# Kernel optimization log

Measured on AMD Instinct MI355X. Metric: run time of the kernel, lower is better.

The kernel has to match this reference:

```python
import jax, jax.numpy as jnp
import numpy as np

B, T, F, H = 8192, 96, 64, 256


def setup_inputs() -> dict:
    key = jax.random.key(0)
    ks = jax.random.split(key, 8)
    s = 0.05
    return {
        "decoder_feature": jax.random.normal(ks[0], (B, T, F), jnp.float32),
        "init_state": jax.random.normal(ks[1], (B, H), jnp.float32),
        "decoder_init_input": jax.random.normal(ks[2], (B, 1), jnp.float32),
        "kernel": jax.random.normal(ks[3], (1 + F, 3 * H), jnp.float32) * s,
        "recurrent_kernel": jax.random.normal(ks[4], (H, 3 * H), jnp.float32) * s,
        "input_bias": jnp.zeros((3 * H,), jnp.float32),
        "recurrent_bias": jnp.zeros((3 * H,), jnp.float32),
        "dense_w": jax.random.normal(ks[5], (H, 1), jnp.float32) * s,
        "dense_b": jnp.zeros((1,), jnp.float32),
        "predict_seq_length": T,
    }


def reference(decoder_feature, init_state, decoder_init_input, kernel,
              recurrent_kernel, input_bias, recurrent_bias, dense_w, dense_b,
              predict_seq_length):
    # teacher=None, use_attention=False path of Decoder2.forward.
    # Keras GRUCell (reset_after=True) recurrence, scanned over time.
    feats = jnp.swapaxes(decoder_feature[:, :predict_seq_length, :], 0, 1)  # [T,B,F]

    def step(carry, feat_t):
        prev_out, h = carry                                   # [B,1], [B,H]
        x = jnp.concatenate([prev_out, feat_t], axis=-1)      # [B,1+F]
        mx = x @ kernel + input_bias                          # [B,3H]
        mh = h @ recurrent_kernel + recurrent_bias            # [B,3H]
        xz, xr, xh = jnp.split(mx, 3, axis=-1)
        hz, hr, hh = jnp.split(mh, 3, axis=-1)
        z = jax.nn.sigmoid(xz + hz)
        r = jax.nn.sigmoid(xr + hr)
        cand = jnp.tanh(xh + r * hh)
        h_new = z * h + (1.0 - z) * cand
        out = h_new @ dense_w + dense_b                       # [B,1]
        return (out, h_new), out

    _, outs = jax.lax.scan(step, (decoder_init_input, init_state), feats)
    return jnp.swapaxes(outs, 0, 1)                           # [B,T,1]
```

## Files before the change

### kernel.cpp

```cpp
#include <hip/hip_runtime.h>


#define Bdim 8192
#define Tdim 96
#define Fdim 64
#define Hdim 256
#define BM   32
#define XS   72
#define HS   264
#define OS   97

typedef __attribute__((ext_vector_type(8))) short s16x8;
typedef __attribute__((ext_vector_type(4))) float f32x4;

#define MFMA __builtin_amdgcn_mfma_f32_16x16x32_bf16

__device__ __forceinline__ unsigned short f2bf(float f) {
    union { float f; unsigned u; } v; v.f = f;
    unsigned r = v.u + 0x7FFFu + ((v.u >> 16) & 1u);
    return (unsigned short)(r >> 16);
}

__device__ __forceinline__ float sigm_fast(float x) {
    return __builtin_amdgcn_rcpf(1.0f + __expf(-x));
}
__device__ __forceinline__ float tanh_fast(float x) {
    return 1.0f - 2.0f * __builtin_amdgcn_rcpf(1.0f + __expf(2.0f * x));
}

__global__ void prep_swz(const float* __restrict__ Wk, const float* __restrict__ Wr,
                         unsigned short* __restrict__ sW) {
    int idx = blockIdx.x * blockDim.x + threadIdx.x;
    if (idx >= 480 * 64) return;
    int lane = idx & 63, f = idx >> 6;
    int n2 = f & 1;
    int g  = (f >> 1) % 3;
    int kt = (f / 6) % 10;
    int w  = f / 60;
    int q = lane >> 4, cc = lane & 15;
    int n = g * 256 + w * 32 + n2 * 16 + cc;
    unsigned short* d = sW + (size_t)idx * 8;
#pragma unroll
    for (int j = 0; j < 8; ++j) {
        float v;
        if (kt < 8) v = Wr[(size_t)(kt * 32 + q * 8 + j) * 768 + n];
        else        v = Wk[(size_t)(1 + (kt - 8) * 32 + q * 8 + j) * 768 + n];
        d[j] = f2bf(v);
    }
}

__launch_bounds__(1024)
__global__ void gru_mfma11(
    const float* __restrict__ feat,
    const float* __restrict__ init_state,
    const float* __restrict__ init_inp,
    const unsigned short* __restrict__ sW,
    const float* __restrict__ Wk,
    const float* __restrict__ ib, const float* __restrict__ rb,
    const float* __restrict__ dw, const float* __restrict__ db,
    float* __restrict__ out)
{
    __shared__ __align__(16) unsigned short xs[2][BM * XS];
    __shared__ __align__(16) unsigned short hs[2][BM * HS];
    __shared__ float wpart[2][16][BM];
    __shared__ float outbuf[BM * OS];

    const int tid  = threadIdx.x;
    const int lane = tid & 63;
    const int wv   = tid >> 6;
    const int q    = lane >> 4;
    const int c    = lane & 15;
    const int b0   = blockIdx.x * BM;
    const int col  = wv * 16 + c;

    const float bz   = ib[col]       + rb[col];
    const float brr  = ib[256 + col] + rb[256 + col];
    const float bxh  = ib[512 + col];
    const float bhh  = rb[512 + col];
    const float wk0z = Wk[col];
    const float wk0r = Wk[256 + col];
    const float wk0h = Wk[512 + col];
    const float dwv  = dw[col];
    const float dbv  = db[0];

    float hreg[2][4];
#pragma unroll
    for (int mt = 0; mt < 2; ++mt)
#pragma unroll
        for (int i = 0; i < 4; ++i) {
            int row = mt * 16 + q * 4 + i;
            float v = init_state[(size_t)(b0 + row) * Hdim + col];
            hreg[mt][i] = v;
            hs[0][row * HS + col] = f2bf(v);
        }

    if (tid < 16 * BM) {
        int ww = tid >> 5, r = tid & 31;
        wpart[1][ww][r] = (ww == 0) ? (init_inp[b0 + r] - dbv) : 0.0f;
    }

    {
        int r = tid >> 5, fi = tid & 31;
        float2 f = *(const float2*)&feat[((size_t)(b0 + r) * Tdim + 0) * Fdim + fi * 2];
        ushort2 p; p.x = f2bf(f.x); p.y = f2bf(f.y);
        *(ushort2*)&xs[0][r * XS + fi * 2] = p;
    }

    const unsigned short* wp0 =
        sW + ((size_t)(wv >> 1) * 60 + (wv & 1)) * 512 + lane * 8;

    __syncthreads();

    for (int t = 0; t < Tdim; ++t) {
        const unsigned short* hsp = hs[t & 1];
        const unsigned short* xsp = xs[t & 1];

        f32x4 az[2], ar[2], ax[2], ah[2];
#pragma unroll
        for (int mt = 0; mt < 2; ++mt) {
            az[mt] = (f32x4)0.0f; ar[mt] = (f32x4)0.0f;
            ax[mt] = (f32x4)0.0f; ah[mt] = (f32x4)0.0f;
        }

#pragma unroll
        for (int kt = 0; kt < 10; ++kt) {
            s16x8 b0f = *(const s16x8*)(wp0 + (size_t)(kt * 3 + 0) * 1024);
            s16x8 b1f = *(const s16x8*)(wp0 + (size_t)(kt * 3 + 1) * 1024);
            s16x8 b2f = *(const s16x8*)(wp0 + (size_t)(kt * 3 + 2) * 1024);
            s16x8 a0, a1;
            if (kt < 8) {
                a0 = *(const s16x8*)&hsp[c * HS + kt * 32 + q * 8];
                a1 = *(const s16x8*)&hsp[(16 + c) * HS + kt * 32 + q * 8];
            } else {
                a0 = *(const s16x8*)&xsp[c * XS + (kt - 8) * 32 + q * 8];
                a1 = *(const s16x8*)&xsp[(16 + c) * XS + (kt - 8) * 32 + q * 8];
            }
            az[0] = MFMA(a0, b0f, az[0], 0, 0, 0);
            az[1] = MFMA(a1, b0f, az[1], 0, 0, 0);
            ar[0] = MFMA(a0, b1f, ar[0], 0, 0, 0);
            ar[1] = MFMA(a1, b1f, ar[1], 0, 0, 0);
            if (kt < 8) {
                ah[0] = MFMA(a0, b2f, ah[0], 0, 0, 0);
                ah[1] = MFMA(a1, b2f, ah[1], 0, 0, 0);
            } else {
                ax[0] = MFMA(a0, b2f, ax[0], 0, 0, 0);
                ax[1] = MFMA(a1, b2f, ax[1], 0, 0, 0);
            }
        }

        float2 fnext;
        int fr = tid >> 5, ffi = tid & 31;
        if (t + 1 < Tdim)
            fnext = *(const float2*)&feat[((size_t)(b0 + fr) * Tdim + (t + 1)) * Fdim + ffi * 2];

        __syncthreads();

        float s;
        {
            int r = lane & 31;
            s = dbv;
            const float (*wp)[BM] = wpart[(t - 1) & 1];
#pragma unroll
            for (int ww = 0; ww < 16; ++ww) s += wp[ww][r];
            if (t > 0 && wv == 0 && lane < 32) outbuf[r * OS + (t - 1)] = s;
        }

        unsigned short* hsn = hs[(t + 1) & 1];
#pragma unroll
        for (int mt = 0; mt < 2; ++mt)
#pragma unroll
            for (int i = 0; i < 4; ++i) {
                float pv = __shfl(s, mt * 16 + q * 4 + i, 64);
                float zz = sigm_fast(az[mt][i] + bz + pv * wk0z);
                float rr = sigm_fast(ar[mt][i] + brr + pv * wk0r);
                float cd = tanh_fast(ax[mt][i] + bxh + pv * wk0h +
                                     rr * (ah[mt][i] + bhh));
                float hn = zz * hreg[mt][i] + (1.0f - zz) * cd;
                hreg[mt][i] = hn;
                hsn[(mt * 16 + q * 4 + i) * HS + col] = f2bf(hn);
                float sp = hn * dwv;
                sp += __shfl_xor(sp, 1, 64);
                sp += __shfl_xor(sp, 2, 64);
                sp += __shfl_xor(sp, 4, 64);
                sp += __shfl_xor(sp, 8, 64);
                if (c == 0) wpart[t & 1][wv][mt * 16 + q * 4 + i] = sp;
            }

        if (t + 1 < Tdim) {
            ushort2 p; p.x = f2bf(fnext.x); p.y = f2bf(fnext.y);
            *(ushort2*)&xs[(t + 1) & 1][fr * XS + ffi * 2] = p;
        }
        __syncthreads();
    }

    {
        int r = lane & 31;
        float s = dbv;
        const float (*wp)[BM] = wpart[(Tdim - 1) & 1];
#pragma unroll
        for (int ww = 0; ww < 16; ++ww) s += wp[ww][r];
        if (wv == 0 && lane < 32) outbuf[r * OS + (Tdim - 1)] = s;
    }
    __syncthreads();

    for (int i = tid; i < BM * Tdim; i += 1024) {
        int r = i / Tdim, tt = i - r * Tdim;
        out[(size_t)b0 * Tdim + i] = outbuf[r * OS + tt];
    }
}

extern "C" void kernel_launch(void* const* d_in, const int* in_sizes, int n_in,
                              void* d_out, int out_size, void* d_ws, size_t ws_size,
                              hipStream_t stream) {
    const float* feat       = (const float*)d_in[0];
    const float* init_state = (const float*)d_in[1];
    const float* init_inp   = (const float*)d_in[2];
    const float* Wk         = (const float*)d_in[3];
    const float* Wr         = (const float*)d_in[4];
    const float* ib         = (const float*)d_in[5];
    const float* rb         = (const float*)d_in[6];
    const float* dw         = (const float*)d_in[7];
    const float* db         = (const float*)d_in[8];
    float* out              = (float*)d_out;

    unsigned short* sW = (unsigned short*)d_ws;

    prep_swz<<<120, 256, 0, stream>>>(Wk, Wr, sW);
    gru_mfma11<<<Bdim / BM, 1024, 0, stream>>>(
        feat, init_state, init_inp, sW, Wk, ib, rb, dw, db, out);
}
```

Measured before the change: 1.831 ms.

## Stage input-weight fragments in LDS, double-buffer recurrent weight loads, drop outbuf

Copies each wave's input-kernel weight fragments into LDS once, so per-step x-side MFMAs read LDS instead of global memory. The recurrent-weight loop now prefetches fragments two k-tiles ahead in registers and runs the x-side MFMAs first to hide global latency. The shared output staging buffer and final copy loop are removed; outputs go straight to global memory as scattered per-step stores. This frees LDS and drops a sync, at the cost of uncoalesced output writes and more register pressure from the prefetch buffers.

```diff
diff --git a/kernel.cpp b/kernel.cpp
--- a/kernel.cpp
+++ b/kernel.cpp
@@ -8,7 +8,6 @@
 #define BM   32
 #define XS   72
 #define HS   264
-#define OS   97
 
 typedef __attribute__((ext_vector_type(8))) short s16x8;
 typedef __attribute__((ext_vector_type(4))) float f32x4;
@@ -50,7 +49,7 @@
 }
 
 __launch_bounds__(1024)
-__global__ void gru_mfma11(
+__global__ void gru_mfma12(
     const float* __restrict__ feat,
     const float* __restrict__ init_state,
     const float* __restrict__ init_inp,
@@ -62,8 +61,8 @@
 {
     __shared__ __align__(16) unsigned short xs[2][BM * XS];
     __shared__ __align__(16) unsigned short hs[2][BM * HS];
+    __shared__ __align__(16) unsigned short wlds[16 * 2 * 3 * 512];
     __shared__ float wpart[2][16][BM];
-    __shared__ float outbuf[BM * OS];
 
     const int tid  = threadIdx.x;
     const int lane = tid & 63;
@@ -109,7 +108,19 @@
     const unsigned short* wp0 =
         sW + ((size_t)(wv >> 1) * 60 + (wv & 1)) * 512 + lane * 8;
 
+    {
+        unsigned short* wld = wlds + (size_t)wv * 3072 + lane * 8;
+#pragma unroll
+        for (int j = 0; j < 2; ++j)
+#pragma unroll
+            for (int g = 0; g < 3; ++g)
+                *(s16x8*)(wld + (j * 3 + g) * 512) =
+                    *(const s16x8*)(wp0 + (size_t)((8 + j) * 3 + g) * 1024);
+    }
+
     __syncthreads();
+
+    const unsigned short* wld = wlds + (size_t)wv * 3072 + lane * 8;
 
     for (int t = 0; t < Tdim; ++t) {
         const unsigned short* hsp = hs[t & 1];
@@ -122,30 +133,48 @@
             ax[mt] = (f32x4)0.0f; ah[mt] = (f32x4)0.0f;
         }
 
-#pragma unroll
-        for (int kt = 0; kt < 10; ++kt) {
-            s16x8 b0f = *(const s16x8*)(wp0 + (size_t)(kt * 3 + 0) * 1024);
-            s16x8 b1f = *(const s16x8*)(wp0 + (size_t)(kt * 3 + 1) * 1024);
-            s16x8 b2f = *(const s16x8*)(wp0 + (size_t)(kt * 3 + 2) * 1024);
-            s16x8 a0, a1;
-            if (kt < 8) {
-                a0 = *(const s16x8*)&hsp[c * HS + kt * 32 + q * 8];
-                a1 = *(const s16x8*)&hsp[(16 + c) * HS + kt * 32 + q * 8];
-            } else {
-                a0 = *(const s16x8*)&xsp[c * XS + (kt - 8) * 32 + q * 8];
-                a1 = *(const s16x8*)&xsp[(16 + c) * XS + (kt - 8) * 32 + q * 8];
+        s16x8 bf[2][3];
+#pragma unroll
+        for (int g = 0; g < 3; ++g)
+            bf[0][g] = *(const s16x8*)(wp0 + (size_t)(0 * 3 + g) * 1024);
+#pragma unroll
+        for (int g = 0; g < 3; ++g)
+            bf[1][g] = *(const s16x8*)(wp0 + (size_t)(1 * 3 + g) * 1024);
+
+#pragma unroll
+        for (int j = 0; j < 2; ++j) {
+            s16x8 w0 = *(const s16x8*)(wld + (j * 3 + 0) * 512);
+            s16x8 w1 = *(const s16x8*)(wld + (j * 3 + 1) * 512);
+            s16x8 w2 = *(const s16x8*)(wld + (j * 3 + 2) * 512);
+            s16x8 a0 = *(const s16x8*)&xsp[c * XS + j * 32 + q * 8];
+            s16x8 a1 = *(const s16x8*)&xsp[(16 + c) * XS + j * 32 + q * 8];
+            az[0] = MFMA(a0, w0, az[0], 0, 0, 0);
+            az[1] = MFMA(a1, w0, az[1], 0, 0, 0);
+            ar[0] = MFMA(a0, w1, ar[0], 0, 0, 0);
+            ar[1] = MFMA(a1, w1, ar[1], 0, 0, 0);
+            ax[0] = MFMA(a0, w2, ax[0], 0, 0, 0);
+            ax[1] = MFMA(a1, w2, ax[1], 0, 0, 0);
+        }
+
+#pragma unroll
+        for (int kt = 0; kt < 8; ++kt) {
+            s16x8 w0 = bf[kt & 1][0];
+            s16x8 w1 = bf[kt & 1][1];
+            s16x8 w2 = bf[kt & 1][2];
+            if (kt + 2 < 8) {
+#pragma unroll
+                for (int g = 0; g < 3; ++g)
+                    bf[kt & 1][g] =
+                        *(const s16x8*)(wp0 + (size_t)((kt + 2) * 3 + g) * 1024);
             }
-            az[0] = MFMA(a0, b0f, az[0], 0, 0, 0);
-            az[1] = MFMA(a1, b0f, az[1], 0, 0, 0);
-            ar[0] = MFMA(a0, b1f, ar[0], 0, 0, 0);
-            ar[1] = MFMA(a1, b1f, ar[1], 0, 0, 0);
-            if (kt < 8) {
-                ah[0] = MFMA(a0, b2f, ah[0], 0, 0, 0);
-                ah[1] = MFMA(a1, b2f, ah[1], 0, 0, 0);
-            } else {
-                ax[0] = MFMA(a0, b2f, ax[0], 0, 0, 0);
-                ax[1] = MFMA(a1, b2f, ax[1], 0, 0, 0);
-            }
+            s16x8 a0 = *(const s16x8*)&hsp[c * HS + kt * 32 + q * 8];
+            s16x8 a1 = *(const s16x8*)&hsp[(16 + c) * HS + kt * 32 + q * 8];
+            az[0] = MFMA(a0, w0, az[0], 0, 0, 0);
+            az[1] = MFMA(a1, w0, az[1], 0, 0, 0);
+            ar[0] = MFMA(a0, w1, ar[0], 0, 0, 0);
+            ar[1] = MFMA(a1, w1, ar[1], 0, 0, 0);
+            ah[0] = MFMA(a0, w2, ah[0], 0, 0, 0);
+            ah[1] = MFMA(a1, w2, ah[1], 0, 0, 0);
         }
 
         float2 fnext;
@@ -162,7 +191,8 @@
             const float (*wp)[BM] = wpart[(t - 1) & 1];
 #pragma unroll
             for (int ww = 0; ww < 16; ++ww) s += wp[ww][r];
-            if (t > 0 && wv == 0 && lane < 32) outbuf[r * OS + (t - 1)] = s;
+            if (t > 0 && wv == 0 && lane < 32)
+                out[(size_t)(b0 + r) * Tdim + (t - 1)] = s;
         }
 
         unsigned short* hsn = hs[(t + 1) & 1];
@@ -199,13 +229,8 @@
         const float (*wp)[BM] = wpart[(Tdim - 1) & 1];
 #pragma unroll
         for (int ww = 0; ww < 16; ++ww) s += wp[ww][r];
-        if (wv == 0 && lane < 32) outbuf[r * OS + (Tdim - 1)] = s;
-    }
-    __syncthreads();
-
-    for (int i = tid; i < BM * Tdim; i += 1024) {
-        int r = i / Tdim, tt = i - r * Tdim;
-        out[(size_t)b0 * Tdim + i] = outbuf[r * OS + tt];
+        if (wv == 0 && lane < 32)
+            out[(size_t)(b0 + r) * Tdim + (Tdim - 1)] = s;
     }
 }
 
@@ -226,6 +251,6 @@
     unsigned short* sW = (unsigned short*)d_ws;
 
     prep_swz<<<120, 256, 0, stream>>>(Wk, Wr, sW);
-    gru_mfma11<<<Bdim / BM, 1024, 0, stream>>>(
+    gru_mfma12<<<Bdim / BM, 1024, 0, stream>>>(
         feat, init_state, init_inp, sW, Wk, ib, rb, dw, db, out);
 }
```

Result: faster. 1.723 ms (-5.9%).

## Stream recurrent weights through LDS ring via async global_load_lds double buffering

Applied to the files above, without the earlier changes.

Each step's weight fragments are now fetched with global_load_lds into a per-wave two-slot LDS ring, two k-tiles ahead, with manual vmcnt/lgkmcnt waits. Before, every k-tile waited on a direct global load. The feature prefetch for the next step is moved ahead of the MFMA loop, and the output staging buffer is dropped in favour of direct global stores each step. This hides global latency in the inner loop but uses more LDS and depends on hand-encoded waitcnt values that must match the number of loads in flight.

```diff
diff --git a/kernel.cpp b/kernel.cpp
--- a/kernel.cpp
+++ b/kernel.cpp
@@ -8,12 +8,20 @@
 #define BM   32
 #define XS   72
 #define HS   264
-#define OS   97
 
 typedef __attribute__((ext_vector_type(8))) short s16x8;
 typedef __attribute__((ext_vector_type(4))) float f32x4;
 
 #define MFMA __builtin_amdgcn_mfma_f32_16x16x32_bf16
+
+#define GLL(gp, lp) __builtin_amdgcn_global_load_lds(                      \
+    (const __attribute__((address_space(1))) void*)(gp),                   \
+    (__attribute__((address_space(3))) void*)(lp), 16, 0, 0)
+
+#define WAIT_VMCNT3 do { __builtin_amdgcn_s_waitcnt(0x0F73);               \
+                         __builtin_amdgcn_sched_barrier(0); } while (0)
+#define WAIT_LGKM0  do { __builtin_amdgcn_s_waitcnt(0xC07F);               \
+                         __builtin_amdgcn_sched_barrier(0); } while (0)
 
 __device__ __forceinline__ unsigned short f2bf(float f) {
     union { float f; unsigned u; } v; v.f = f;
@@ -50,7 +58,7 @@
 }
 
 __launch_bounds__(1024)
-__global__ void gru_mfma11(
+__global__ void gru_mfma15(
     const float* __restrict__ feat,
     const float* __restrict__ init_state,
     const float* __restrict__ init_inp,
@@ -62,8 +70,8 @@
 {
     __shared__ __align__(16) unsigned short xs[2][BM * XS];
     __shared__ __align__(16) unsigned short hs[2][BM * HS];
+    __shared__ __align__(16) unsigned short wring[16 * 2 * 3 * 512];
     __shared__ float wpart[2][16][BM];
-    __shared__ float outbuf[BM * OS];
 
     const int tid  = threadIdx.x;
     const int lane = tid & 63;
@@ -108,6 +116,14 @@
 
     const unsigned short* wp0 =
         sW + ((size_t)(wv >> 1) * 60 + (wv & 1)) * 512 + lane * 8;
+    const int rbase = wv * 3072;
+
+#pragma unroll
+    for (int k0 = 0; k0 < 2; ++k0)
+#pragma unroll
+        for (int g = 0; g < 3; ++g)
+            GLL(wp0 + (size_t)(k0 * 3 + g) * 1024,
+                &wring[rbase + k0 * 1536 + g * 512]);
 
     __syncthreads();
 
@@ -115,6 +131,11 @@
         const unsigned short* hsp = hs[t & 1];
         const unsigned short* xsp = xs[t & 1];
 
+        float2 fnext;
+        int fr = tid >> 5, ffi = tid & 31;
+        if (t + 1 < Tdim)
+            fnext = *(const float2*)&feat[((size_t)(b0 + fr) * Tdim + (t + 1)) * Fdim + ffi * 2];
+
         f32x4 az[2], ar[2], ax[2], ah[2];
 #pragma unroll
         for (int mt = 0; mt < 2; ++mt) {
@@ -124,9 +145,13 @@
 
 #pragma unroll
         for (int kt = 0; kt < 10; ++kt) {
-            s16x8 b0f = *(const s16x8*)(wp0 + (size_t)(kt * 3 + 0) * 1024);
-            s16x8 b1f = *(const s16x8*)(wp0 + (size_t)(kt * 3 + 1) * 1024);
-            s16x8 b2f = *(const s16x8*)(wp0 + (size_t)(kt * 3 + 2) * 1024);
+            const int slot = kt & 1;
+            WAIT_VMCNT3;
+
+            const unsigned short* bs = &wring[rbase + slot * 1536 + lane * 8];
+            s16x8 w0 = *(const s16x8*)(bs + 0 * 512);
+            s16x8 w1 = *(const s16x8*)(bs + 1 * 512);
+            s16x8 w2 = *(const s16x8*)(bs + 2 * 512);
             s16x8 a0, a1;
             if (kt < 8) {
                 a0 = *(const s16x8*)&hsp[c * HS + kt * 32 + q * 8];
@@ -135,23 +160,28 @@
                 a0 = *(const s16x8*)&xsp[c * XS + (kt - 8) * 32 + q * 8];
                 a1 = *(const s16x8*)&xsp[(16 + c) * XS + (kt - 8) * 32 + q * 8];
             }
-            az[0] = MFMA(a0, b0f, az[0], 0, 0, 0);
-            az[1] = MFMA(a1, b0f, az[1], 0, 0, 0);
-            ar[0] = MFMA(a0, b1f, ar[0], 0, 0, 0);
-            ar[1] = MFMA(a1, b1f, ar[1], 0, 0, 0);
+
+            WAIT_LGKM0;
+            {
+                const int ktn = (kt + 2) % 10;
+#pragma unroll
+                for (int g = 0; g < 3; ++g)
+                    GLL(wp0 + (size_t)(ktn * 3 + g) * 1024,
+                        &wring[rbase + slot * 1536 + g * 512]);
+            }
+
+            az[0] = MFMA(a0, w0, az[0], 0, 0, 0);
+            az[1] = MFMA(a1, w0, az[1], 0, 0, 0);
+            ar[0] = MFMA(a0, w1, ar[0], 0, 0, 0);
+            ar[1] = MFMA(a1, w1, ar[1], 0, 0, 0);
             if (kt < 8) {
-                ah[0] = MFMA(a0, b2f, ah[0], 0, 0, 0);
-                ah[1] = MFMA(a1, b2f, ah[1], 0, 0, 0);
+                ah[0] = MFMA(a0, w2, ah[0], 0, 0, 0);
+                ah[1] = MFMA(a1, w2, ah[1], 0, 0, 0);
             } else {
-                ax[0] = MFMA(a0, b2f, ax[0], 0, 0, 0);
-                ax[1] = MFMA(a1, b2f, ax[1], 0, 0, 0);
-            }
-        }
-
-        float2 fnext;
-        int fr = tid >> 5, ffi = tid & 31;
-        if (t + 1 < Tdim)
-            fnext = *(const float2*)&feat[((size_t)(b0 + fr) * Tdim + (t + 1)) * Fdim + ffi * 2];
+                ax[0] = MFMA(a0, w2, ax[0], 0, 0, 0);
+                ax[1] = MFMA(a1, w2, ax[1], 0, 0, 0);
+            }
+        }
 
         __syncthreads();
 
@@ -162,7 +192,8 @@
             const float (*wp)[BM] = wpart[(t - 1) & 1];
 #pragma unroll
             for (int ww = 0; ww < 16; ++ww) s += wp[ww][r];
-            if (t > 0 && wv == 0 && lane < 32) outbuf[r * OS + (t - 1)] = s;
+            if (t > 0 && wv == 0 && lane < 32)
+                out[(size_t)(b0 + r) * Tdim + (t - 1)] = s;
         }
 
         unsigned short* hsn = hs[(t + 1) & 1];
@@ -199,13 +230,8 @@
         const float (*wp)[BM] = wpart[(Tdim - 1) & 1];
 #pragma unroll
         for (int ww = 0; ww < 16; ++ww) s += wp[ww][r];
-        if (wv == 0 && lane < 32) outbuf[r * OS + (Tdim - 1)] = s;
-    }
-    __syncthreads();
-
-    for (int i = tid; i < BM * Tdim; i += 1024) {
-        int r = i / Tdim, tt = i - r * Tdim;
-        out[(size_t)b0 * Tdim + i] = outbuf[r * OS + tt];
+        if (wv == 0 && lane < 32)
+            out[(size_t)(b0 + r) * Tdim + (Tdim - 1)] = s;
     }
 }
 
@@ -226,6 +252,6 @@
     unsigned short* sW = (unsigned short*)d_ws;
 
     prep_swz<<<120, 256, 0, stream>>>(Wk, Wr, sW);
-    gru_mfma11<<<Bdim / BM, 1024, 0, stream>>>(
+    gru_mfma15<<<Bdim / BM, 1024, 0, stream>>>(
         feat, init_state, init_inp, sW, Wk, ib, rb, dw, db, out);
 }
```

New measurement: 1.682 ms. 8.2% less time.
